# Performance work log

Measured on AMD Instinct MI355X. Metric: run time of the kernel, lower is better.

Reference implementation:

```python
import jax, jax.numpy as jnp
import numpy as np

N_NODES = 100000
N_EDGES = 400000
D_IN = 128
D_OUT = 128
BN_EPS = 1e-5


def setup_inputs() -> dict:
    key = jax.random.key(0)
    ks = jax.random.split(key, 9)
    node_feats = jax.random.normal(ks[0], (N_NODES, D_IN), dtype=jnp.float32)
    src = jax.random.randint(ks[1], (N_EDGES,), 0, N_NODES)
    dst = jax.random.randint(ks[2], (N_EDGES,), 0, N_NODES)
    # GraphConv weight/bias
    W = jax.random.normal(ks[3], (D_IN, D_OUT), dtype=jnp.float32) * (1.0 / np.sqrt(D_IN))
    b = jax.random.normal(ks[4], (D_OUT,), dtype=jnp.float32) * 0.01
    # residual Linear weight/bias
    Wr = jax.random.normal(ks[5], (D_IN, D_OUT), dtype=jnp.float32) * (1.0 / np.sqrt(D_IN))
    br = jax.random.normal(ks[6], (D_OUT,), dtype=jnp.float32) * 0.01
    # BatchNorm1d affine params
    gamma = jnp.ones((D_OUT,), dtype=jnp.float32) + 0.1 * jax.random.normal(ks[7], (D_OUT,), dtype=jnp.float32)
    beta = 0.1 * jax.random.normal(ks[8], (D_OUT,), dtype=jnp.float32)
    return {"node_feats": node_feats, "W": W, "b": b, "Wr": Wr, "br": br,
            "gamma": gamma, "beta": beta, "src": src, "dst": dst}


def reference(node_feats, W, b, Wr, br, gamma, beta, src, dst):
    ones_e = jnp.ones((src.shape[0],), dtype=node_feats.dtype)
    out_deg = jax.ops.segment_sum(ones_e, src, num_segments=N_NODES)
    in_deg = jax.ops.segment_sum(ones_e, dst, num_segments=N_NODES)
    # norm='both': D_out^{-1/2} on source side, D_in^{-1/2} on dest side (clamp 0-degree)
    c_src = jax.lax.rsqrt(jnp.maximum(out_deg, 1.0))  # [N]
    c_dst = jax.lax.rsqrt(jnp.maximum(in_deg, 1.0))   # [N]
    x_scaled = node_feats * c_src[:, None]            # [N, D_in]
    msgs = x_scaled[src]                              # gather -> [E, D_in]
    agg = jax.ops.segment_sum(msgs, dst, num_segments=N_NODES)  # scatter-add -> [N, D_in]
    h = agg * c_dst[:, None]
    h = jax.nn.relu(h @ W + b)                        # GraphConv activation
    res = jax.nn.relu(node_feats @ Wr + br)           # residual branch
    y = h + res
    # BatchNorm1d, training mode: batch stats, biased variance
    mean = jnp.mean(y, axis=0)
    var = jnp.mean(jnp.square(y - mean), axis=0)
    y_hat = (y - mean) * jax.lax.rsqrt(var + BN_EPS)
    return y_hat * gamma + beta
```

## Files before the change

kernel.cpp:

```cpp
#include <hip/hip_runtime.h>

#define N_NODES 100000
#define N_EDGES 400000
#define D 128
#define BN_EPS 1e-5f
#define NTILES 6250

typedef short short8 __attribute__((ext_vector_type(8)));
typedef float f32x4 __attribute__((ext_vector_type(4)));

static __device__ __forceinline__ float bf2f(unsigned short u) {
    unsigned x = ((unsigned)u) << 16;
    return __builtin_bit_cast(float, x);
}
static __device__ __forceinline__ unsigned short f2bf(float f) {
    unsigned x = __builtin_bit_cast(unsigned, f);
    x += 0x7fffu + ((x >> 16) & 1u);
    return (unsigned short)(x >> 16);
}
static __device__ __forceinline__ void splitbf(float a, short& hi, short& lo) {
    unsigned short h = f2bf(a);
    float r = a - bf2f(h);
    hi = (short)h;
    lo = (short)f2bf(r);
}
static __device__ __forceinline__ void split2(float a, float b, unsigned& hiw, unsigned& low) {
    short ha, la, hb, lb;
    splitbf(a, ha, la);
    splitbf(b, hb, lb);
    hiw = (unsigned)(unsigned short)ha | ((unsigned)(unsigned short)hb << 16);
    low = (unsigned)(unsigned short)la | ((unsigned)(unsigned short)lb << 16);
}
static __device__ __forceinline__ void split8(f32x4 a, f32x4 b, uint4& hi, uint4& lo) {
    unsigned h0, h1, h2, h3, l0, l1, l2, l3;
    split2(a[0], a[1], h0, l0);
    split2(a[2], a[3], h1, l1);
    split2(b[0], b[1], h2, l2);
    split2(b[2], b[3], h3, l3);
    hi = uint4{h0, h1, h2, h3};
    lo = uint4{l0, l1, l2, l3};
}

__global__ void k_zero_out(float* __restrict__ y, int n4) {
    int t = blockIdx.x * blockDim.x + threadIdx.x;
    if (t < n4) ((float4*)y)[t] = float4{0.f, 0.f, 0.f, 0.f};
}

__global__ void k_count(const int* __restrict__ src, const int* __restrict__ dst,
                        int* __restrict__ cnt_src, int* __restrict__ cnt_dst) {
    int t = blockIdx.x * blockDim.x + threadIdx.x;
    if (t >= N_EDGES) return;
    atomicAdd(&cnt_src[src[t]], 1);
    atomicAdd(&cnt_dst[dst[t]], 1);
}

__global__ void k_scan1(const int* __restrict__ cnt, int* __restrict__ outp,
                        int* __restrict__ bsum,
                        const int* __restrict__ cnt_src,
                        float* __restrict__ c_src, float* __restrict__ c_dst,
                        int* __restrict__ fill) {
    __shared__ int s[256];
    int i = blockIdx.x * 256 + threadIdx.x;
    int v = (i < N_NODES) ? cnt[i] : 0;
    if (i < N_NODES) {
        c_src[i] = rsqrtf(fmaxf((float)cnt_src[i], 1.0f));
        c_dst[i] = rsqrtf(fmaxf((float)v, 1.0f));
        fill[i] = 0;
    }
    s[threadIdx.x] = v;
    __syncthreads();
    for (int d = 1; d < 256; d <<= 1) {
        int t = (threadIdx.x >= d) ? s[threadIdx.x - d] : 0;
        __syncthreads();
        s[threadIdx.x] += t;
        __syncthreads();
    }
    if (i < N_NODES) outp[i] = s[threadIdx.x] - v;
    if (threadIdx.x == 255) bsum[blockIdx.x] = s[255];
}

__global__ void k_scan2(int* __restrict__ bsum, int nb) {
    __shared__ int s[512];
    int v = (threadIdx.x < nb) ? bsum[threadIdx.x] : 0;
    s[threadIdx.x] = v;
    __syncthreads();
    for (int d = 1; d < 512; d <<= 1) {
        int t = (threadIdx.x >= d) ? s[threadIdx.x - d] : 0;
        __syncthreads();
        s[threadIdx.x] += t;
        __syncthreads();
    }
    if (threadIdx.x < nb) bsum[threadIdx.x] = s[threadIdx.x] - v;
}

__global__ void k_scan3(int* __restrict__ rowStart, const int* __restrict__ boff) {
    int i = blockIdx.x * 256 + threadIdx.x;
    if (i < N_NODES) rowStart[i] += boff[i >> 8];
    if (i == 0) rowStart[N_NODES] = N_EDGES;
}

__global__ void k_fill(const int* __restrict__ src, const int* __restrict__ dst,
                       const int* __restrict__ rowStart, int* __restrict__ fill,
                       int* __restrict__ esorted) {
    int e = blockIdx.x * blockDim.x + threadIdx.x;
    if (e >= N_EDGES) return;
    int d = dst[e];
    int pos = rowStart[d] + atomicAdd(&fill[d], 1);
    esorted[pos] = src[e];
}

__global__ void k_make_frags(const float* __restrict__ W,
                             const float* __restrict__ Wr,
                             unsigned short* __restrict__ Whi, unsigned short* __restrict__ Wlo,
                             unsigned short* __restrict__ Wrhi, unsigned short* __restrict__ Wrlo) {
    int t = blockIdx.x * blockDim.x + threadIdx.x;
    if (t >= 4096) return;
    int mat = t >> 11;
    int fragIdx = (t >> 6) & 31;
    int lane = t & 63;
    int nt = fragIdx >> 2, ks = fragIdx & 3;
    const float* Wsrc = mat ? Wr : W;
    unsigned short* dhi = mat ? Wrhi : Whi;
    unsigned short* dlo = mat ? Wrlo : Wlo;
    int n = nt * 16 + (lane & 15);
    int kbase = ks * 32 + (lane >> 4) * 8;
    short hi[8], lo[8];
#pragma unroll
    for (int j = 0; j < 8; j++) splitbf(Wsrc[(kbase + j) * D + n], hi[j], lo[j]);
    ((uint4*)dhi)[fragIdx * 64 + lane] = *(uint4*)hi;
    ((uint4*)dlo)[fragIdx * 64 + lane] = *(uint4*)lo;
}

__global__ __launch_bounds__(256, 2) void k_fused(
    const float* __restrict__ x,
    const int* __restrict__ esorted, const int* __restrict__ rowStart,
    const float* __restrict__ c_src, const float* __restrict__ c_dst,
    const unsigned short* __restrict__ Whi, const unsigned short* __restrict__ Wlo,
    const unsigned short* __restrict__ Wrhi, const unsigned short* __restrict__ Wrlo,
    const float* __restrict__ bias_h, const float* __restrict__ bias_r,
    float* __restrict__ yout,
    float* __restrict__ gsum, float* __restrict__ gsq) {
    __shared__ uint4 A[2][16][64];

    const int wave = threadIdx.x >> 6;
    const int lane = threadIdx.x & 63;
    const int quad = lane >> 4;
    const int l16 = lane & 15;

    short8 wHf[8], wLf[8], rHf[8], rLf[8];
#pragma unroll
    for (int f = 0; f < 8; f++) {
        int nt = wave * 2 + (f >> 2), ks = f & 3;
        int gi = (nt * 4 + ks) * 64 + lane;
        wHf[f] = __builtin_bit_cast(short8, ((const uint4*)Whi)[gi]);
        wLf[f] = __builtin_bit_cast(short8, ((const uint4*)Wlo)[gi]);
        rHf[f] = __builtin_bit_cast(short8, ((const uint4*)Wrhi)[gi]);
        rLf[f] = __builtin_bit_cast(short8, ((const uint4*)Wrlo)[gi]);
    }
    float bh[2], brr[2];
#pragma unroll
    for (int ntl = 0; ntl < 2; ntl++) {
        int col = wave * 32 + ntl * 16 + l16;
        bh[ntl] = bias_h[col];
        brr[ntl] = bias_r[col];
    }

    float s_acc[2] = {0.f, 0.f}, q_acc[2] = {0.f, 0.f};
    const f32x4* __restrict__ xb = (const f32x4*)x;

    int buf = 0;
    for (int rt = blockIdx.x; rt < NTILES; rt += gridDim.x, buf ^= 1) {
        const int rowbase = rt * 16;

        {
            const int R = wave * 4 + quad;
            const int n = rowbase + R;
            const int li = l16;
            const int beg = rowStart[n], end = rowStart[n + 1];
            f32x4 X0 = xb[(size_t)n * 32 + li * 2], X1 = xb[(size_t)n * 32 + li * 2 + 1];
            f32x4 A0 = {0.f, 0.f, 0.f, 0.f}, A1 = {0.f, 0.f, 0.f, 0.f};
            for (int j = beg; j < end; j += 8) {
                int idx[8];
                float c[8];
                f32x4 pa[8], pb[8];
#pragma unroll
                for (int k = 0; k < 8; k++) {
                    int jj = j + k;
                    idx[k] = esorted[(jj < end) ? jj : j];
                }
#pragma unroll
                for (int k = 0; k < 8; k++)
                    c[k] = (j + k < end) ? c_src[idx[k]] : 0.f;
#pragma unroll
                for (int k = 0; k < 8; k++) {
                    pa[k] = xb[(size_t)idx[k] * 32 + li * 2];
                    pb[k] = xb[(size_t)idx[k] * 32 + li * 2 + 1];
                }
#pragma unroll
                for (int k = 0; k < 8; k++) {
                    A0 += pa[k] * c[k];
                    A1 += pb[k] * c[k];
                }
            }
            float cd = c_dst[n];
            A0 *= cd; A1 *= cd;
            uint4 ahi, alo, xhi, xlo;
            split8(A0, A1, ahi, alo);
            split8(X0, X1, xhi, xlo);
            uint4* Arow = &A[buf][R][0];
            const int sw = li ^ (R & 7);
            Arow[sw] = ahi;
            Arow[16 + sw] = alo;
            Arow[32 + sw] = xhi;
            Arow[48 + sw] = xlo;
        }
        __syncthreads();

        const uint4* rowA = &A[buf][l16][0];
        const int r7 = l16 & 7;
        short8 aH[4], aL[4], xH[4], xL[4];
#pragma unroll
        for (int ks = 0; ks < 4; ks++) {
            const int sl = (ks * 4 + quad) ^ r7;
            aH[ks] = __builtin_bit_cast(short8, rowA[sl]);
            aL[ks] = __builtin_bit_cast(short8, rowA[16 + sl]);
            xH[ks] = __builtin_bit_cast(short8, rowA[32 + sl]);
            xL[ks] = __builtin_bit_cast(short8, rowA[48 + sl]);
        }

        f32x4 accH[2], accR[2];
#pragma unroll
        for (int ntl = 0; ntl < 2; ntl++) {
            accH[ntl] = f32x4{0.f, 0.f, 0.f, 0.f};
            accR[ntl] = f32x4{0.f, 0.f, 0.f, 0.f};
#pragma unroll
            for (int ks = 0; ks < 4; ks++) {
                const int f = ntl * 4 + ks;
                accH[ntl] = __builtin_amdgcn_mfma_f32_16x16x32_bf16(aH[ks], wHf[f], accH[ntl], 0, 0, 0);
                accH[ntl] = __builtin_amdgcn_mfma_f32_16x16x32_bf16(aH[ks], wLf[f], accH[ntl], 0, 0, 0);
                accH[ntl] = __builtin_amdgcn_mfma_f32_16x16x32_bf16(aL[ks], wHf[f], accH[ntl], 0, 0, 0);
                accR[ntl] = __builtin_amdgcn_mfma_f32_16x16x32_bf16(xH[ks], rHf[f], accR[ntl], 0, 0, 0);
                accR[ntl] = __builtin_amdgcn_mfma_f32_16x16x32_bf16(xH[ks], rLf[f], accR[ntl], 0, 0, 0);
                accR[ntl] = __builtin_amdgcn_mfma_f32_16x16x32_bf16(xL[ks], rHf[f], accR[ntl], 0, 0, 0);
            }
        }

#pragma unroll
        for (int ntl = 0; ntl < 2; ntl++) {
            float s = 0.f, q = 0.f;
#pragma unroll
            for (int r = 0; r < 4; r++) {
                float y = fmaxf(accH[ntl][r] + bh[ntl], 0.f) + fmaxf(accR[ntl][r] + brr[ntl], 0.f);
                yout[(size_t)(rowbase + quad * 4 + r) * D + wave * 32 + ntl * 16 + l16] = y;
                s += y;
                q += y * y;
            }
            s_acc[ntl] += s;
            q_acc[ntl] += q;
        }
    }

#pragma unroll
    for (int ntl = 0; ntl < 2; ntl++) {
        float s = s_acc[ntl], q = q_acc[ntl];
        s += __shfl_xor(s, 16, 64);
        s += __shfl_xor(s, 32, 64);
        q += __shfl_xor(q, 16, 64);
        q += __shfl_xor(q, 32, 64);
        if (lane < 16) {
            unsafeAtomicAdd(&gsum[wave * 32 + ntl * 16 + lane], s);
            unsafeAtomicAdd(&gsq[wave * 32 + ntl * 16 + lane], q);
        }
    }
}

__global__ void k_bn_apply(float* __restrict__ y,
                           const float* __restrict__ gsum, const float* __restrict__ gsq,
                           const float* __restrict__ gamma, const float* __restrict__ beta) {
    __shared__ float sc[128], sh[128];
    if (threadIdx.x < 128) {
        int f = threadIdx.x;
        const float invN = 1.0f / (float)N_NODES;
        float mean = gsum[f] * invN;
        float var = fmaxf(gsq[f] * invN - mean * mean, 0.f);
        float s = gamma[f] * rsqrtf(var + BN_EPS);
        sc[f] = s;
        sh[f] = beta[f] - mean * s;
    }
    __syncthreads();
    const int total4 = N_NODES * D / 4;
    for (int i = blockIdx.x * blockDim.x + threadIdx.x; i < total4; i += gridDim.x * blockDim.x) {
        float4 v = ((float4*)y)[i];
        int f = (i * 4) & (D - 1);
        v.x = v.x * sc[f] + sh[f];
        v.y = v.y * sc[f + 1] + sh[f + 1];
        v.z = v.z * sc[f + 2] + sh[f + 2];
        v.w = v.w * sc[f + 3] + sh[f + 3];
        ((float4*)y)[i] = v;
    }
}

extern "C" void kernel_launch(void* const* d_in, const int* in_sizes, int n_in,
                              void* d_out, int out_size, void* d_ws, size_t ws_size,
                              hipStream_t stream) {
    const float* x     = (const float*)d_in[0];
    const float* W     = (const float*)d_in[1];
    const float* b     = (const float*)d_in[2];
    const float* Wr    = (const float*)d_in[3];
    const float* br    = (const float*)d_in[4];
    const float* gamma = (const float*)d_in[5];
    const float* beta  = (const float*)d_in[6];
    const int* src = (const int*)d_in[7];
    const int* dst = (const int*)d_in[8];
    float* out = (float*)d_out;

    const int NB1 = (N_NODES + 255) / 256;

    char* ws = (char*)d_ws;
    size_t off = 0;
    float* gsum    = (float*)(ws + off); off += 512;
    float* gsq     = (float*)(ws + off); off += 512;
    int* cnt_src   = (int*)(ws + off); off += 400128;
    int* cnt_dst   = (int*)(ws + off); off += 400128;
    const size_t zero_bytes = off;
    int* fill      = (int*)(ws + off); off += 400128;
    int* rowStart  = (int*)(ws + off); off += 400384;
    int* bsum      = (int*)(ws + off); off += 2048;
    int* esorted   = (int*)(ws + off); off += (size_t)N_EDGES * 4;
    float* c_src   = (float*)(ws + off); off += 400128;
    float* c_dst   = (float*)(ws + off); off += 400128;
    unsigned short* WhiF  = (unsigned short*)(ws + off); off += 32768;
    unsigned short* WloF  = (unsigned short*)(ws + off); off += 32768;
    unsigned short* WrhiF = (unsigned short*)(ws + off); off += 32768;
    unsigned short* WrloF = (unsigned short*)(ws + off); off += 32768;
    const size_t needed = off;

    if (ws_size < needed) {
        k_zero_out<<<(N_NODES * D / 4 + 255) / 256, 256, 0, stream>>>(out, N_NODES * D / 4);
        return;
    }

    hipMemsetAsync(d_ws, 0, zero_bytes, stream);

    k_make_frags<<<16, 256, 0, stream>>>(W, Wr, WhiF, WloF, WrhiF, WrloF);
    k_count<<<(N_EDGES + 255) / 256, 256, 0, stream>>>(src, dst, cnt_src, cnt_dst);
    k_scan1<<<NB1, 256, 0, stream>>>(cnt_dst, rowStart, bsum, cnt_src, c_src, c_dst, fill);
    k_scan2<<<1, 512, 0, stream>>>(bsum, NB1);
    k_scan3<<<NB1, 256, 0, stream>>>(rowStart, bsum);
    k_fill<<<(N_EDGES + 255) / 256, 256, 0, stream>>>(src, dst, rowStart, fill, esorted);
    k_fused<<<1024, 256, 0, stream>>>(x, esorted, rowStart, c_src, c_dst,
                                      WhiF, WloF, WrhiF, WrloF, b, br, out, gsum, gsq);
    k_bn_apply<<<2048, 256, 0, stream>>>(out, gsum, gsq, gamma, beta);
}
```

Measured before the change: 248.3 us.

## Fuse scan kernels into cooperative launch and fold memset into frag kernel

Replaces the three-kernel prefix scan over destination counts with a single cooperative kernel that uses grid syncs between the block scan, block-sum scan and offset add. It also drops the hipMemsetAsync by zeroing the count arrays inside the weight-fragment kernel and zeroing the BN accumulators inside the scan. The aim is fewer launches and less inter-kernel gap overhead. It adds grid-sync cost and depends on cooperative launch support, keeping the old path as a fallback.

```diff
diff --git a/kernel.cpp b/kernel.cpp
--- a/kernel.cpp
+++ b/kernel.cpp
@@ -1,10 +1,13 @@
 #include <hip/hip_runtime.h>
+#include <hip/hip_cooperative_groups.h>
 
 #define N_NODES 100000
 #define N_EDGES 400000
 #define D 128
 #define BN_EPS 1e-5f
 #define NTILES 6250
+#define NINTS 100032
+#define SCB 196
 
 typedef short short8 __attribute__((ext_vector_type(8)));
 typedef float f32x4 __attribute__((ext_vector_type(4)));
@@ -54,66 +57,16 @@
     atomicAdd(&cnt_dst[dst[t]], 1);
 }
 
-__global__ void k_scan1(const int* __restrict__ cnt, int* __restrict__ outp,
-                        int* __restrict__ bsum,
-                        const int* __restrict__ cnt_src,
-                        float* __restrict__ c_src, float* __restrict__ c_dst,
-                        int* __restrict__ fill) {
-    __shared__ int s[256];
-    int i = blockIdx.x * 256 + threadIdx.x;
-    int v = (i < N_NODES) ? cnt[i] : 0;
-    if (i < N_NODES) {
-        c_src[i] = rsqrtf(fmaxf((float)cnt_src[i], 1.0f));
-        c_dst[i] = rsqrtf(fmaxf((float)v, 1.0f));
-        fill[i] = 0;
-    }
-    s[threadIdx.x] = v;
-    __syncthreads();
-    for (int d = 1; d < 256; d <<= 1) {
-        int t = (threadIdx.x >= d) ? s[threadIdx.x - d] : 0;
-        __syncthreads();
-        s[threadIdx.x] += t;
-        __syncthreads();
-    }
-    if (i < N_NODES) outp[i] = s[threadIdx.x] - v;
-    if (threadIdx.x == 255) bsum[blockIdx.x] = s[255];
-}
-
-__global__ void k_scan2(int* __restrict__ bsum, int nb) {
-    __shared__ int s[512];
-    int v = (threadIdx.x < nb) ? bsum[threadIdx.x] : 0;
-    s[threadIdx.x] = v;
-    __syncthreads();
-    for (int d = 1; d < 512; d <<= 1) {
-        int t = (threadIdx.x >= d) ? s[threadIdx.x - d] : 0;
-        __syncthreads();
-        s[threadIdx.x] += t;
-        __syncthreads();
-    }
-    if (threadIdx.x < nb) bsum[threadIdx.x] = s[threadIdx.x] - v;
-}
-
-__global__ void k_scan3(int* __restrict__ rowStart, const int* __restrict__ boff) {
-    int i = blockIdx.x * 256 + threadIdx.x;
-    if (i < N_NODES) rowStart[i] += boff[i >> 8];
-    if (i == 0) rowStart[N_NODES] = N_EDGES;
-}
-
-__global__ void k_fill(const int* __restrict__ src, const int* __restrict__ dst,
-                       const int* __restrict__ rowStart, int* __restrict__ fill,
-                       int* __restrict__ esorted) {
-    int e = blockIdx.x * blockDim.x + threadIdx.x;
-    if (e >= N_EDGES) return;
-    int d = dst[e];
-    int pos = rowStart[d] + atomicAdd(&fill[d], 1);
-    esorted[pos] = src[e];
-}
-
 __global__ void k_make_frags(const float* __restrict__ W,
                              const float* __restrict__ Wr,
                              unsigned short* __restrict__ Whi, unsigned short* __restrict__ Wlo,
-                             unsigned short* __restrict__ Wrhi, unsigned short* __restrict__ Wrlo) {
+                             unsigned short* __restrict__ Wrhi, unsigned short* __restrict__ Wrlo,
+                             int* __restrict__ cnt_src, int* __restrict__ cnt_dst) {
     int t = blockIdx.x * blockDim.x + threadIdx.x;
+    for (int i = t; i < NINTS; i += 131072) {
+        cnt_src[i] = 0;
+        cnt_dst[i] = 0;
+    }
     if (t >= 4096) return;
     int mat = t >> 11;
     int fragIdx = (t >> 6) & 31;
@@ -129,6 +82,107 @@
     for (int j = 0; j < 8; j++) splitbf(Wsrc[(kbase + j) * D + n], hi[j], lo[j]);
     ((uint4*)dhi)[fragIdx * 64 + lane] = *(uint4*)hi;
     ((uint4*)dlo)[fragIdx * 64 + lane] = *(uint4*)lo;
+}
+
+__global__ void k_scan_all(const int* __restrict__ cnt_dst, int* __restrict__ rowStart,
+                           int* __restrict__ bsum,
+                           const int* __restrict__ cnt_src,
+                           float* __restrict__ c_src, float* __restrict__ c_dst,
+                           int* __restrict__ fill,
+                           float* __restrict__ gsum, float* __restrict__ gsq) {
+    __shared__ int s[512];
+    const int i = blockIdx.x * 512 + threadIdx.x;
+    int v = (i < N_NODES) ? cnt_dst[i] : 0;
+    if (i < N_NODES) {
+        c_src[i] = rsqrtf(fmaxf((float)cnt_src[i], 1.0f));
+        c_dst[i] = rsqrtf(fmaxf((float)v, 1.0f));
+        fill[i] = 0;
+    }
+    if (i < 128) { gsum[i] = 0.f; gsq[i] = 0.f; }
+    s[threadIdx.x] = v;
+    __syncthreads();
+    for (int d = 1; d < 512; d <<= 1) {
+        int t = (threadIdx.x >= d) ? s[threadIdx.x - d] : 0;
+        __syncthreads();
+        s[threadIdx.x] += t;
+        __syncthreads();
+    }
+    if (i < N_NODES) rowStart[i] = s[threadIdx.x] - v;
+    if (threadIdx.x == 511) bsum[blockIdx.x] = s[511];
+    cooperative_groups::this_grid().sync();
+    if (blockIdx.x == 0) {
+        int v2 = (threadIdx.x < SCB) ? bsum[threadIdx.x] : 0;
+        __syncthreads();
+        s[threadIdx.x] = v2;
+        __syncthreads();
+        for (int d = 1; d < 512; d <<= 1) {
+            int t = (threadIdx.x >= d) ? s[threadIdx.x - d] : 0;
+            __syncthreads();
+            s[threadIdx.x] += t;
+            __syncthreads();
+        }
+        if (threadIdx.x < SCB) bsum[threadIdx.x] = s[threadIdx.x] - v2;
+    }
+    cooperative_groups::this_grid().sync();
+    if (i < N_NODES) rowStart[i] += bsum[i >> 9];
+    if (i == 0) rowStart[N_NODES] = N_EDGES;
+}
+
+__global__ void k_scan1(const int* __restrict__ cnt, int* __restrict__ outp,
+                        int* __restrict__ bsum,
+                        const int* __restrict__ cnt_src,
+                        float* __restrict__ c_src, float* __restrict__ c_dst,
+                        int* __restrict__ fill,
+                        float* __restrict__ gsum, float* __restrict__ gsq) {
+    __shared__ int s[256];
+    int i = blockIdx.x * 256 + threadIdx.x;
+    int v = (i < N_NODES) ? cnt[i] : 0;
+    if (i < N_NODES) {
+        c_src[i] = rsqrtf(fmaxf((float)cnt_src[i], 1.0f));
+        c_dst[i] = rsqrtf(fmaxf((float)v, 1.0f));
+        fill[i] = 0;
+    }
+    if (i < 128) { gsum[i] = 0.f; gsq[i] = 0.f; }
+    s[threadIdx.x] = v;
+    __syncthreads();
+    for (int d = 1; d < 256; d <<= 1) {
+        int t = (threadIdx.x >= d) ? s[threadIdx.x - d] : 0;
+        __syncthreads();
+        s[threadIdx.x] += t;
+        __syncthreads();
+    }
+    if (i < N_NODES) outp[i] = s[threadIdx.x] - v;
+    if (threadIdx.x == 255) bsum[blockIdx.x] = s[255];
+}
+
+__global__ void k_scan2(int* __restrict__ bsum, int nb) {
+    __shared__ int s[512];
+    int v = (threadIdx.x < nb) ? bsum[threadIdx.x] : 0;
+    s[threadIdx.x] = v;
+    __syncthreads();
+    for (int d = 1; d < 512; d <<= 1) {
+        int t = (threadIdx.x >= d) ? s[threadIdx.x - d] : 0;
+        __syncthreads();
+        s[threadIdx.x] += t;
+        __syncthreads();
+    }
+    if (threadIdx.x < nb) bsum[threadIdx.x] = s[threadIdx.x] - v;
+}
+
+__global__ void k_scan3(int* __restrict__ rowStart, const int* __restrict__ boff) {
+    int i = blockIdx.x * 256 + threadIdx.x;
+    if (i < N_NODES) rowStart[i] += boff[i >> 8];
+    if (i == 0) rowStart[N_NODES] = N_EDGES;
+}
+
+__global__ void k_fill(const int* __restrict__ src, const int* __restrict__ dst,
+                       const int* __restrict__ rowStart, int* __restrict__ fill,
+                       int* __restrict__ esorted) {
+    int e = blockIdx.x * blockDim.x + threadIdx.x;
+    if (e >= N_EDGES) return;
+    int d = dst[e];
+    int pos = rowStart[d] + atomicAdd(&fill[d], 1);
+    esorted[pos] = src[e];
 }
 
 __global__ __launch_bounds__(256, 2) void k_fused(
@@ -322,7 +376,6 @@
     float* gsq     = (float*)(ws + off); off += 512;
     int* cnt_src   = (int*)(ws + off); off += 400128;
     int* cnt_dst   = (int*)(ws + off); off += 400128;
-    const size_t zero_bytes = off;
     int* fill      = (int*)(ws + off); off += 400128;
     int* rowStart  = (int*)(ws + off); off += 400384;
     int* bsum      = (int*)(ws + off); off += 2048;
@@ -340,13 +393,23 @@
         return;
     }
 
-    hipMemsetAsync(d_ws, 0, zero_bytes, stream);
-
-    k_make_frags<<<16, 256, 0, stream>>>(W, Wr, WhiF, WloF, WrhiF, WrloF);
+    k_make_frags<<<512, 256, 0, stream>>>(W, Wr, WhiF, WloF, WrhiF, WrloF, cnt_src, cnt_dst);
     k_count<<<(N_EDGES + 255) / 256, 256, 0, stream>>>(src, dst, cnt_src, cnt_dst);
-    k_scan1<<<NB1, 256, 0, stream>>>(cnt_dst, rowStart, bsum, cnt_src, c_src, c_dst, fill);
-    k_scan2<<<1, 512, 0, stream>>>(bsum, NB1);
-    k_scan3<<<NB1, 256, 0, stream>>>(rowStart, bsum);
+    {
+        void* sargs[] = {
+            (void*)&cnt_dst, (void*)&rowStart, (void*)&bsum, (void*)&cnt_src,
+            (void*)&c_src, (void*)&c_dst, (void*)&fill, (void*)&gsum, (void*)&gsq
+        };
+        hipError_t ce = hipLaunchCooperativeKernel((const void*)k_scan_all, dim3(SCB), dim3(512),
+                                                   sargs, 0, stream);
+        if (ce != hipSuccess) {
+            (void)hipGetLastError();
+            k_scan1<<<NB1, 256, 0, stream>>>(cnt_dst, rowStart, bsum, cnt_src,
+                                             c_src, c_dst, fill, gsum, gsq);
+            k_scan2<<<1, 512, 0, stream>>>(bsum, NB1);
+            k_scan3<<<NB1, 256, 0, stream>>>(rowStart, bsum);
+        }
+    }
     k_fill<<<(N_EDGES + 255) / 256, 256, 0, stream>>>(src, dst, rowStart, fill, esorted);
     k_fused<<<1024, 256, 0, stream>>>(x, esorted, rowStart, c_src, c_dst,
                                       WhiF, WloF, WrhiF, WrloF, b, br, out, gsum, gsq);
```

Measured after the change: 306.6 us. 1.24x slower.
